# Optimization experiments

Measured on AMD Instinct MI355X. Metric: run time of the kernel, lower is better.

The kernel has to match this reference:

```python
import jax, jax.numpy as jnp
import numpy as np
from jax import lax

B, CIN, HF, WF = 8, 512, 60, 60      # encoder feature
NCLS = 19                            # seg out channels
PATCH = 10                           # patch_size
DEPTH = 8                            # 2**att_depth
UPS = 8                              # seg upsampling
HI = HF * UPS                        # 480 upsampled image size
NP_IMG = (HI // PATCH) ** 2          # 2304 image patches
NP_FEA = (HI // DEPTH // PATCH) ** 2 # 36 feature patches
POOL_SIZES = (1, 2, 3, 6)


def resize_ac(x, H, W):
    # bilinear, align_corners=True (matches F.interpolate/UpsamplingBilinear2d)
    b, c, h, w = x.shape
    ys = jnp.arange(H, dtype=x.dtype) * ((h - 1) / max(H - 1, 1))
    xs = jnp.arange(W, dtype=x.dtype) * ((w - 1) / max(W - 1, 1))
    y0 = jnp.floor(ys).astype(jnp.int32); y1 = jnp.minimum(y0 + 1, h - 1)
    x0 = jnp.floor(xs).astype(jnp.int32); x1 = jnp.minimum(x0 + 1, w - 1)
    wy = (ys - y0.astype(x.dtype))[:, None]
    wx = (xs - x0.astype(x.dtype))[None, :]
    g = lambda yi, xi: x[:, :, yi[:, None], xi[None, :]]
    top = (1 - wx) * g(y0, x0) + wx * g(y0, x1)
    bot = (1 - wx) * g(y1, x0) + wx * g(y1, x1)
    return (1 - wy) * top + wy * bot


def bn_eval(x, gamma, beta, mean, var, eps=1e-5):
    s = lambda v: v[None, :, None, None]
    return (x - s(mean)) * (s(gamma) / jnp.sqrt(s(var) + eps)) + s(beta)


def setup_inputs() -> dict:
    key = jax.random.key(0)
    ks = jax.random.split(key, 16)
    f32 = jnp.float32
    return {
        "feat": jax.random.normal(ks[0], (B, CIN, HF, WF), f32),
        "attentions": jax.random.normal(ks[1], (B, NCLS, NP_IMG, NP_FEA), f32),
        "w_psp": jax.random.normal(ks[2], (4, CIN // 4, CIN), f32) * 0.03,
        "b_psp0": jax.random.normal(ks[3], (CIN // 4,), f32) * 0.02,
        "bn_psp_gamma": jax.random.uniform(ks[4], (3, CIN // 4), f32, 0.5, 1.5),
        "bn_psp_beta": jax.random.normal(ks[5], (3, CIN // 4), f32) * 0.02,
        "bn_psp_mean": jax.random.normal(ks[6], (3, CIN // 4), f32) * 0.02,
        "bn_psp_var": jax.random.uniform(ks[7], (3, CIN // 4), f32, 0.5, 1.5),
        "w_conv": jax.random.normal(ks[8], (512, 2 * CIN), f32) * 0.03,
        "bn_conv_gamma": jax.random.uniform(ks[9], (512,), f32, 0.5, 1.5),
        "bn_conv_beta": jax.random.normal(ks[10], (512,), f32) * 0.02,
        "bn_conv_mean": jax.random.normal(ks[11], (512,), f32) * 0.02,
        "bn_conv_var": jax.random.uniform(ks[12], (512,), f32, 0.5, 1.5),
        "w_segconv": jax.random.normal(ks[13], (NCLS, 512, 3, 3), f32) * 0.03,
        "b_segconv": jax.random.normal(ks[14], (NCLS,), f32) * 0.02,
    }


def _forward(feat, attentions, w_psp, b_psp0, bn_psp_gamma, bn_psp_beta,
             bn_psp_mean, bn_psp_var, w_conv, bn_conv_gamma, bn_conv_beta,
             bn_conv_mean, bn_conv_var, w_segconv, b_segconv):
    # ---- PSP pyramid ----
    branches = []
    for i, p in enumerate(POOL_SIZES):
        k = HF // p
        pooled = feat.reshape(B, CIN, p, k, p, k).mean(axis=(3, 5))  # adaptive avg pool
        y = jnp.einsum('oc,bchw->bohw', w_psp[i], pooled)
        if i == 0:  # pool_size==1 -> no BN, conv has bias
            y = y + b_psp0[None, :, None, None]
        else:
            y = bn_eval(y, bn_psp_gamma[i-1], bn_psp_beta[i-1],
                        bn_psp_mean[i-1], bn_psp_var[i-1])
        y = jax.nn.relu(y)
        branches.append(resize_ac(y, HF, WF))
    x = jnp.concatenate(branches + [feat], axis=1)  # [B, 2*CIN, HF, WF]

    # ---- 1x1 Conv2dReLU + BN (eval), dropout is identity in eval ----
    x = jnp.einsum('oc,bchw->bohw', w_conv, x)
    x = jax.nn.relu(bn_eval(x, bn_conv_gamma, bn_conv_beta, bn_conv_mean, bn_conv_var))

    # ---- SegmentationHead ----
    x = lax.conv_general_dilated(x, w_segconv, (1, 1), 'SAME',
                                 dimension_numbers=('NCHW', 'OIHW', 'NCHW'))
    x = x + b_segconv[None, :, None, None]
    x = resize_ac(x, HI, HI)  # [B, NCLS, 480, 480]

    # one-hot of per-pixel argmax (scatter of ones)
    am = jnp.argmax(x, axis=1)
    x_softmax = (am[:, None] == jnp.arange(NCLS)[None, :, None, None]).astype(x.dtype)

    # grouped ones-conv stride 8 / 64 == 8x8 average pooling
    hf = HI // DEPTH  # 60
    argx_feamap = x_softmax.reshape(B, NCLS, hf, DEPTH, hf, DEPTH).mean(axis=(3, 5))

    # unfold(k=10, s=10): [B, C, 36, 100] (blocks row-major, patch row-major)
    nb = hf // PATCH  # 6
    unf = argx_feamap.reshape(B, NCLS, nb, PATCH, nb, PATCH)
    unf = unf.transpose(0, 1, 2, 4, 3, 5).reshape(B, NCLS, nb * nb, PATCH * PATCH)

    counts = jnp.count_nonzero(attentions, axis=-1, keepdims=True).astype(x.dtype) + 1e-5
    att = jnp.einsum('bcpk,bckq->bcpq', attentions / counts, unf)  # [B,C,2304,100]

    # fold back to [B, C, 480, 480]
    nbi = HI // PATCH  # 48
    corr = att.reshape(B, NCLS, nbi, nbi, PATCH, PATCH)
    corr = corr.transpose(0, 1, 2, 4, 3, 5).reshape(B, NCLS, HI, HI)

    x = corr * x + x  # activation=None -> identity
    return x, attentions


def reference(feat, attentions, w_psp, b_psp0, bn_psp_gamma, bn_psp_beta,
              bn_psp_mean, bn_psp_var, w_conv, bn_conv_gamma, bn_conv_beta,
              bn_conv_mean, bn_conv_var, w_segconv, b_segconv):
    return _forward(feat, attentions, w_psp, b_psp0, bn_psp_gamma, bn_psp_beta,
                    bn_psp_mean, bn_psp_var, w_conv, bn_conv_gamma, bn_conv_beta,
                    bn_conv_mean, bn_conv_var, w_segconv, b_segconv)
```

## Files before the change

### kernel.cpp

```cpp
#include <hip/hip_runtime.h>
#include <stdint.h>

#define NB 8
#define NCLS 19

typedef short s8v __attribute__((ext_vector_type(8)));
typedef float f4v __attribute__((ext_vector_type(4)));

__device__ __forceinline__ unsigned short f2b(float f){
  union { float f; uint32_t u; } v; v.f = f;
  uint32_t u = v.u;
  uint32_t r = (u + 0x7fffu + ((u >> 16) & 1u)) >> 16;
  return (unsigned short)r;
}

#define GLOAD16(g, l) __builtin_amdgcn_global_load_lds( \
    (const __attribute__((address_space(1))) unsigned int*)(g), \
    (__attribute__((address_space(3))) unsigned int*)(l), 16, 0, 0)

#define OFF_X512 0
#define OFF_POOL 31490048
#define OFF_Z    32309248
#define OFF_BNS  33128448
#define OFF_BNB  33130496
#define OFF_SEG  33132544
#define OFF_ARGX 35321344
#define OFF_WSEG 37510144
#define OFF_WF   37805056

__global__ __launch_bounds__(256) void k_setup(
    const float* __restrict__ feat, unsigned short* __restrict__ featT,
    unsigned short* __restrict__ x512p,
    const float* __restrict__ wseg, unsigned short* __restrict__ wsegT,
    const float* __restrict__ wconv, unsigned short* __restrict__ wfT,
    const float* __restrict__ g, const float* __restrict__ be,
    const float* __restrict__ m, const float* __restrict__ v,
    float* __restrict__ sc, float* __restrict__ sh,
    unsigned short* __restrict__ argxT, float* __restrict__ pooled)
{
  __shared__ unsigned short lt[64*528];
  int bid = blockIdx.x;
  if (bid < 456){
    int b = bid / 57, px0 = (bid - b*57)*64;
    for (int i = threadIdx.x; i < 64*512; i += 256){
      int c = i >> 6, px = i & 63;
      float val = feat[((size_t)b*512 + c)*3600 + min(px0+px, 3599)];
      lt[px*528 + c] = f2b(val);
    }
    __syncthreads();
    for (int i = threadIdx.x; i < 4096; i += 256){
      int px = i >> 6, c8 = i & 63;
      s8v vv = *(const s8v*)(lt + px*528 + c8*8);
      *(s8v*)(featT + ((size_t)b*3712 + px0 + px)*512 + c8*8) = vv;
    }
    return;
  }
  bid -= 456;
  if (bid < 488){
    int idx = bid*256 + threadIdx.x;
    if (idx < 124928){
      int pix = idx >> 6;
      int ch  = (idx & 63) << 3;
      int b = pix / 244;
      int r = pix - b*244;
      int h, w;
      if (r < 62){ h = 0; w = r; }
      else if (r < 124){ h = 61; w = r - 62; }
      else if (r < 184){ h = r - 124 + 1; w = 0; }
      else { h = r - 184 + 1; w = 61; }
      s8v z = (s8v){0,0,0,0,0,0,0,0};
      *(s8v*)(x512p + (((size_t)b*62 + h)*62 + w)*512 + ch) = z;
    }
    return;
  }
  bid -= 488;
  if (bid < 576){
    int idx = bid*256 + threadIdx.x;
    if (idx < 9*32*512){
      int tap = idx / (32*512);
      int rem = idx - tap*(32*512);
      int o = rem >> 9, c = rem & 511;
      float val = (o < NCLS) ? wseg[((size_t)o*512 + c)*9 + tap] : 0.0f;
      wsegT[idx] = f2b(val);
    }
    return;
  }
  bid -= 576;
  if (bid < 1024){
    int idx = bid*256 + threadIdx.x;
    if (idx < 512*512){
      int o = idx >> 9, c = idx & 511;
      wfT[idx] = f2b(wconv[(size_t)o*1024 + 512 + c]);
    }
    return;
  }
  bid -= 1024;
  if (bid < 2){
    int i = bid*256 + threadIdx.x;
    if (i < 512){
      float s = g[i] * rsqrtf(v[i] + 1e-5f);
      sc[i] = s; sh[i] = be[i] - m[i]*s;
    }
    return;
  }
  bid -= 2;
  if (bid < 532){
    int gi = bid*256 + threadIdx.x;
    if (gi < 136192){
      s8v z = (s8v){0,0,0,0,0,0,0,0};
      ((s8v*)argxT)[gi] = z;
    }
    return;
  }
  bid -= 532;
  {
    int w = threadIdx.x >> 6, lane = threadIdx.x & 63;
    int bc = bid*4 + w;
    float* rs = (float*)lt + w*64*12;
    if (lane < 60){
      const float* row = feat + (size_t)bc*3600 + lane*60;
      float s6[6];
      #pragma unroll
      for (int j = 0; j < 6; j++){
        float s = 0.f;
        #pragma unroll
        for (int i = 0; i < 10; i++) s += row[j*10+i];
        s6[j] = s;
      }
      float s3_0 = s6[0]+s6[1], s3_1 = s6[2]+s6[3], s3_2 = s6[4]+s6[5];
      float s2_0 = s3_0 + s6[2], s2_1 = s6[3] + s3_2;
      rs[lane*12+0] = s2_0 + s2_1;
      rs[lane*12+1] = s2_0; rs[lane*12+2] = s2_1;
      rs[lane*12+3] = s3_0; rs[lane*12+4] = s3_1; rs[lane*12+5] = s3_2;
      #pragma unroll
      for (int j = 0; j < 6; j++) rs[lane*12+6+j] = s6[j];
    }
    __syncthreads();
    if (lane < 50){
      int P, by, bx, jcol;
      if (lane == 0){ P=1; by=0; bx=0; jcol=0; }
      else if (lane < 5){ P=2; int l=lane-1; by=l>>1; bx=l&1; jcol=1+bx; }
      else if (lane < 14){ P=3; int l=lane-5; by=l/3; bx=l-(l/3)*3; jcol=3+bx; }
      else { P=6; int l=lane-14; by=l/6; bx=l-(l/6)*6; jcol=6+bx; }
      int k = 60/P;
      float s = 0.f;
      for (int rr = 0; rr < k; rr++) s += rs[(by*k+rr)*12 + jcol];
      pooled[(size_t)bc*50 + lane] = s * (1.0f/((float)k*(float)k));
    }
  }
}

__global__ __launch_bounds__(256) void k2_branch(
    const float* __restrict__ pooled, const float* __restrict__ w_psp,
    const float* __restrict__ b_psp0,
    const float* __restrict__ png, const float* __restrict__ pnb,
    const float* __restrict__ pnm, const float* __restrict__ pnv,
    const float* __restrict__ wconv, float* __restrict__ zbuf)
{
  int bin = blockIdx.x % 50;
  int b   = blockIdx.x / 50;
  int br  = (bin < 1) ? 0 : (bin < 5) ? 1 : (bin < 14) ? 2 : 3;
  __shared__ float pl[512];
  __shared__ float ysh[128];
  int t = threadIdx.x;
  pl[t]       = pooled[((size_t)b*512 + t)*50 + bin];
  pl[t + 256] = pooled[((size_t)b*512 + t + 256)*50 + bin];
  __syncthreads();
  if (t < 128){
    const float* wr = w_psp + ((size_t)br*128 + t)*512;
    float s = 0.f;
    #pragma unroll 8
    for (int c = 0; c < 512; c++) s += pl[c]*wr[c];
    if (br == 0) s += b_psp0[t];
    else {
      int ib = (br-1)*128 + t;
      s = (s - pnm[ib]) * png[ib] * rsqrtf(pnv[ib] + 1e-5f) + pnb[ib];
    }
    ysh[t] = fmaxf(s, 0.f);
  }
  __syncthreads();
  for (int o = t; o < 512; o += 256){
    const float* wc = wconv + (size_t)o*1024 + br*128;
    float s = 0.f;
    #pragma unroll
    for (int c = 0; c < 128; c++) s += ysh[c]*wc[c];
    zbuf[((size_t)b*50 + bin)*512 + o] = s;
  }
}

__global__ __launch_bounds__(256) void k3_gemm(
    const unsigned short* __restrict__ featT, const unsigned short* __restrict__ wfT,
    const float* __restrict__ zbuf, const float* __restrict__ bns,
    const float* __restrict__ bnb, unsigned short* __restrict__ x512p)
{
  __shared__ unsigned short lmem[2*128*64];
  unsigned short* lA = lmem;
  unsigned short* lB = lmem + 128*64;

  const int t = threadIdx.x;
  const int lane = t & 63;
  const int wave = t >> 6;
  const int wm = wave >> 1;
  const int wn = wave & 1;
  const int pix0 = blockIdx.x * 128;
  const int o0   = blockIdx.y * 128;
  const int b    = blockIdx.z;

  f4v acc[4][4];
  #pragma unroll
  for (int i = 0; i < 4; i++)
    #pragma unroll
    for (int j = 0; j < 4; j++)
      acc[i][j] = (f4v){0.f,0.f,0.f,0.f};

  const int sub  = lane >> 3;
  const int slot = lane & 7;

  for (int kk = 0; kk < 8; kk++){
    #pragma unroll
    for (int j = 0; j < 4; j++){
      int px = j*32 + wave*8 + sub;
      int pix = min(pix0 + px, 3599);
      const unsigned short* src = featT + ((size_t)b*3712 + pix)*512 + kk*64 + ((slot ^ (px & 7)) << 3);
      GLOAD16(src, lA + j*2048 + wave*512);
    }
    #pragma unroll
    for (int j = 0; j < 4; j++){
      int o = j*32 + wave*8 + sub;
      const unsigned short* src = wfT + (size_t)(o0 + o)*512 + kk*64 + ((slot ^ (o & 7)) << 3);
      GLOAD16(src, lB + j*2048 + wave*512);
    }
    __syncthreads();
    #pragma unroll
    for (int ks = 0; ks < 2; ks++){
      const int chunk = ks*4 + (lane >> 4);
      s8v af[4], bg[4];
      #pragma unroll
      for (int mf = 0; mf < 4; mf++){
        int p = wm*64 + mf*16 + (lane & 15);
        af[mf] = *(s8v*)((char*)lA + p*128 + ((chunk ^ (p & 7)))*16);
      }
      #pragma unroll
      for (int nf = 0; nf < 4; nf++){
        int o = wn*64 + nf*16 + (lane & 15);
        bg[nf] = *(s8v*)((char*)lB + o*128 + ((chunk ^ (o & 7)))*16);
      }
      #pragma unroll
      for (int mf = 0; mf < 4; mf++)
        #pragma unroll
        for (int nf = 0; nf < 4; nf++)
          acc[mf][nf] = __builtin_amdgcn_mfma_f32_16x16x32_bf16(af[mf], bg[nf], acc[mf][nf], 0, 0, 0);
    }
    __syncthreads();
  }

  float* zl  = (float*)lmem;
  float* lsc = zl + 50*128;
  float* lsh = lsc + 128;
  for (int i = t; i < 50*128; i += 256){
    int bin = i >> 7, ol = i & 127;
    zl[i] = zbuf[((size_t)b*50 + bin)*512 + o0 + ol];
  }
  if (t < 128){ lsc[t] = bns[o0 + t]; lsh[t] = bnb[o0 + t]; }
  __syncthreads();

  #pragma unroll
  for (int mf = 0; mf < 4; mf++){
    #pragma unroll
    for (int r = 0; r < 4; r++){
      int p = pix0 + wm*64 + mf*16 + (lane >> 4)*4 + r;
      if (p >= 3600) continue;
      int h = p / 60, w = p - (p/60)*60;
      float wgt[3][4]; int bix[3][4];
      const int pbase[3] = {1,5,14};
      const int psz[3]   = {2,3,6};
      #pragma unroll
      for (int ib = 0; ib < 3; ib++){
        int P = psz[ib];
        float fy = (float)h * (float)(P-1) / 59.0f;
        float fx = (float)w * (float)(P-1) / 59.0f;
        int y0 = (int)fy; int y1 = min(y0+1, P-1); float wy = fy - (float)y0;
        int x0 = (int)fx; int x1 = min(x0+1, P-1); float wx = fx - (float)x0;
        bix[ib][0] = pbase[ib] + y0*P + x0; wgt[ib][0] = (1.f-wy)*(1.f-wx);
        bix[ib][1] = pbase[ib] + y0*P + x1; wgt[ib][1] = (1.f-wy)*wx;
        bix[ib][2] = pbase[ib] + y1*P + x0; wgt[ib][2] = wy*(1.f-wx);
        bix[ib][3] = pbase[ib] + y1*P + x1; wgt[ib][3] = wy*wx;
      }
      size_t obase = (((size_t)b*62 + (h+1))*62 + (w+1))*512 + o0;
      #pragma unroll
      for (int nf = 0; nf < 4; nf++){
        int ol = wn*64 + nf*16 + (lane & 15);
        float zs = zl[ol];
        #pragma unroll
        for (int ib = 0; ib < 3; ib++)
          #pragma unroll
          for (int tp = 0; tp < 4; tp++)
            zs += wgt[ib][tp] * zl[bix[ib][tp]*128 + ol];
        float v = acc[mf][nf][r] + zs;
        v = fmaxf(v * lsc[ol] + lsh[ol], 0.f);
        x512p[obase + ol] = f2b(v);
      }
    }
  }
}

__global__ __launch_bounds__(256) void k4_conv(
    const unsigned short* __restrict__ x512p, const unsigned short* __restrict__ wsegT,
    const float* __restrict__ bseg, float* __restrict__ seg60)
{
  __shared__ unsigned short lW[32*512];
  const int h = blockIdx.x;
  const int b = blockIdx.y;
  const int t = threadIdx.x;
  const int lane = t & 63;
  const int wave = t >> 6;
  const int wpix = wave*16 + (lane & 15);
  const int wld = min(wpix, 59);

  f4v acc[2];
  acc[0] = (f4v){0.f,0.f,0.f,0.f};
  acc[1] = (f4v){0.f,0.f,0.f,0.f};

  for (int tap = 0; tap < 9; tap++){
    __syncthreads();
    for (int i = t; i < 2048; i += 256){
      int orow = i >> 6;
      int cn = i & 63;
      s8v v = *(const s8v*)(wsegT + ((size_t)tap*32 + orow)*512 + cn*8);
      *(s8v*)((char*)lW + orow*1024 + ((cn ^ (orow & 7)))*16) = v;
    }
    __syncthreads();
    int dy = tap/3 - 1, dx = tap - (tap/3)*3 - 1;
    const unsigned short* arow = x512p + (((size_t)b*62 + (h+dy+1))*62 + (wld+dx+1))*512 + (lane>>4)*8;
    #pragma unroll 4
    for (int cs = 0; cs < 16; cs++){
      int cb = cs*32;
      s8v a = *(const s8v*)(arow + cb);
      #pragma unroll
      for (int nf = 0; nf < 2; nf++){
        int o = nf*16 + (lane & 15);
        int chunk = (cb >> 3) + (lane >> 4);
        s8v bv = *(s8v*)((char*)lW + o*1024 + ((chunk ^ (o & 7)))*16);
        acc[nf] = __builtin_amdgcn_mfma_f32_16x16x32_bf16(a, bv, acc[nf], 0, 0, 0);
      }
    }
  }
  #pragma unroll
  for (int nf = 0; nf < 2; nf++){
    int o = nf*16 + (lane & 15);
    if (o < NCLS){
      float bias = bseg[o];
      #pragma unroll
      for (int r = 0; r < 4; r++){
        int wst = wave*16 + (lane >> 4)*4 + r;
        if (wst < 60)
          seg60[(((size_t)b*60 + h)*60 + wst)*NCLS + o] = acc[nf][r] + bias;
      }
    }
  }
}

__global__ __launch_bounds__(256) void k5_argmax(const float* __restrict__ seg60, unsigned short* __restrict__ argxT){
  int fy = blockIdx.x, b = blockIdx.y;
  __shared__ float L[3*60*20];
  int ylo;
  { float yy0 = (float)(fy*8) * (59.0f/479.0f); ylo = (int)yy0; }
  for (int i = threadIdx.x; i < 3600; i += 256){
    int r = i/1200, rem = i - r*1200, x = rem/20, c = rem - x*20;
    int row = min(ylo + r, 59);
    L[i] = (c < 19) ? seg60[(((size_t)b*60 + row)*60 + x)*NCLS + c] : -3.0e38f;
  }
  __syncthreads();
  int wave = threadIdx.x >> 6, lane = threadIdx.x & 63;
  int py = fy*8 + (lane >> 3), lpx = lane & 7;
  float yy = (float)py * (59.0f/479.0f); int y0 = (int)yy; int y1 = min(y0+1, 59); float wy = yy - (float)y0;
  const float* r0 = L + (y0 - ylo)*1200;
  const float* r1 = L + (y1 - ylo)*1200;
  #pragma unroll 3
  for (int pass = 0; pass < 15; pass++){
    int fx = pass*4 + wave;
    int px = fx*8 + lpx;
    float xx = (float)px * (59.0f/479.0f); int x0 = (int)xx; int x1 = min(x0+1, 59); float wx = xx - (float)x0;
    float w00 = (1.f-wy)*(1.f-wx), w01 = (1.f-wy)*wx, w10 = wy*(1.f-wx), w11 = wy*wx;
    const float* s00 = r0 + x0*20; const float* s01 = r0 + x1*20;
    const float* s10 = r1 + x0*20; const float* s11 = r1 + x1*20;
    float best = -3.0e38f; int bc = 0;
    #pragma unroll
    for (int c = 0; c < NCLS; c++){
      float v = w00*s00[c] + w01*s01[c] + w10*s10[c] + w11*s11[c];
      if (v > best){ best = v; bc = c; }
    }
    int cnt = 0;
    #pragma unroll
    for (int c = 0; c < NCLS; c++){
      unsigned long long m = __ballot(bc == c);
      if (lane == c) cnt = __popcll(m);
    }
    int ky = fy/10, qy = fy - (fy/10)*10, kx = fx/10, qx = fx - (fx/10)*10;
    int q = qy*10 + qx, k = ky*6 + kx;
    if (lane < NCLS){
      unsigned short hv = f2b((float)cnt * (1.0f/64.0f));
      argxT[(size_t)(b*NCLS + lane)*7168 + q*64 + (((k>>3) ^ (q&7))<<3) + (k&7)] = hv;
    }
  }
}

__global__ __launch_bounds__(256) void k7_final(
    const float* __restrict__ att, const unsigned short* __restrict__ argxT,
    const float* __restrict__ seg60, float* __restrict__ out, float* __restrict__ out2)
{
  int pr = blockIdx.x, c = blockIdx.y, b = blockIdx.z;
  __shared__ char pool[22720];
  unsigned short* Abf = (unsigned short*)pool;
  unsigned short* Ubf = (unsigned short*)(pool + 6144);
  float* corrl = (float*)pool;
  float* inv   = (float*)(pool + 21504);
  float* srow  = (float*)(pool + 21696);
  const int t = threadIdx.x;
  const int lane = t & 63;
  const int wave = t >> 6;

  int ybase; { float yy0 = (float)(pr*10)*(59.0f/479.0f); ybase = (int)yy0; }

  const size_t aoff = (((size_t)b*NCLS + c)*2304 + (size_t)pr*48)*36;
  const float* ab = att + aoff;
  float* o2 = out2 + aoff;
  for (int i = t; i < 768; i += 256){
    int pc = i >> 4, j = i & 15;
    ushort4 w4 = make_ushort4(0,0,0,0);
    if (j < 9){
      f4v v = *(const f4v*)(ab + pc*36 + j*4);
      *(f4v*)(o2 + pc*36 + j*4) = v;
      w4.x = f2b(v[0]); w4.y = f2b(v[1]); w4.z = f2b(v[2]); w4.w = f2b(v[3]);
    }
    int ch = j >> 1;
    *(ushort4*)((char*)Abf + pc*128 + (((ch ^ (pc & 7)))<<4) + (j & 1)*8) = w4;
  }
  {
    const unsigned short* up = argxT + (size_t)(b*NCLS + c)*7168;
    #pragma unroll
    for (int r = 0; r < 4; r++){
      int chunk0 = r*256 + wave*64;
      if (chunk0 < 896)
        GLOAD16(up + (size_t)(chunk0 + lane)*8, Ubf + (size_t)chunk0*8);
    }
  }
  if (t < 240){
    int j = t/60, x = t - (t/60)*60;
    int row = min(ybase + j, 59);
    srow[j*64 + x] = seg60[(((size_t)b*60 + row)*60 + x)*NCLS + c];
  }
  if (t < 48){
    int nz = 0;
    #pragma unroll
    for (int j2 = 0; j2 < 9; j2++){
      f4v v = *(const f4v*)(ab + t*36 + j2*4);
      nz += (v[0]!=0.f)+(v[1]!=0.f)+(v[2]!=0.f)+(v[3]!=0.f);
    }
    inv[t] = 1.0f/((float)nz + 1e-5f);
  }
  __syncthreads();

  f4v acc[6];
  #pragma unroll
  for (int s = 0; s < 6; s++) acc[s] = (f4v){0.f,0.f,0.f,0.f};
  #pragma unroll
  for (int s = 0; s < 6; s++){
    int pi = wave + s*4;
    if (pi < 21){
      int M = pi/7, N = pi - (pi/7)*7;
      #pragma unroll
      for (int ks = 0; ks < 2; ks++){
        int chunk = ks*4 + (lane >> 4);
        int ar = M*16 + (lane & 15);
        s8v af = *(s8v*)((char*)Abf + ar*128 + ((chunk ^ (ar & 7))<<4));
        int qr = N*16 + (lane & 15);
        s8v bg = *(s8v*)((char*)Ubf + qr*128 + ((chunk ^ (qr & 7))<<4));
        acc[s] = __builtin_amdgcn_mfma_f32_16x16x32_bf16(af, bg, acc[s], 0, 0, 0);
      }
    }
  }
  float hA[4], hB[4];
  {
    float xxa = (float)t * (59.0f/479.0f);
    int xa0 = (int)xxa; int xa1 = min(xa0+1, 59); float wxa = xxa - (float)xa0;
    int px2 = t + 256;
    float xxb = (float)px2 * (59.0f/479.0f);
    int xb0 = (int)xxb; int xb1 = min(xb0+1, 59); float wxb = xxb - (float)xb0;
    #pragma unroll
    for (int j = 0; j < 4; j++){
      hA[j] = (1.f-wxa)*srow[j*64 + xa0] + wxa*srow[j*64 + xa1];
      hB[j] = (px2 < 480) ? ((1.f-wxb)*srow[j*64 + xb0] + wxb*srow[j*64 + xb1]) : 0.f;
    }
  }
  __syncthreads();

  #pragma unroll
  for (int s = 0; s < 6; s++){
    int pi = wave + s*4;
    if (pi < 21){
      int M = pi/7, N = pi - (pi/7)*7;
      int q = N*16 + (lane & 15);
      #pragma unroll
      for (int r = 0; r < 4; r++){
        int pc = M*16 + (lane >> 4)*4 + r;
        corrl[pc*112 + q] = acc[s][r] * inv[pc];
      }
    }
  }
  __syncthreads();

  float* outb = out + ((size_t)b*NCLS + c)*230400 + (size_t)pr*4800;
  int pcA = (t*6554) >> 16, qxA = t - pcA*10;
  int px2 = t + 256;
  int pcB = (px2*6554) >> 16, qxB = px2 - pcB*10;
  #pragma unroll
  for (int qy = 0; qy < 10; qy++){
    int py = pr*10 + qy;
    float yy = (float)py * (59.0f/479.0f);
    int y0 = (int)yy; int y1 = min(y0+1, 59); float wy = yy - (float)y0;
    int j0 = y0 - ybase, j1 = y1 - ybase;
    float h0a = (j0==0)?hA[0]:(j0==1)?hA[1]:(j0==2)?hA[2]:hA[3];
    float h1a = (j1==0)?hA[0]:(j1==1)?hA[1]:(j1==2)?hA[2]:hA[3];
    float omw = 1.f - wy;
    float xv = omw*h0a + wy*h1a;
    outb[qy*480 + t] = xv * (1.f + corrl[pcA*112 + qy*10 + qxA]);
    if (px2 < 480){
      float h0b = (j0==0)?hB[0]:(j0==1)?hB[1]:(j0==2)?hB[2]:hB[3];
      float h1b = (j1==0)?hB[0]:(j1==1)?hB[1]:(j1==2)?hB[2]:hB[3];
      float xv2 = omw*h0b + wy*h1b;
      outb[qy*480 + px2] = xv2 * (1.f + corrl[pcB*112 + qy*10 + qxB]);
    }
  }
}

extern "C" void kernel_launch(void* const* d_in, const int* in_sizes, int n_in,
                              void* d_out, int out_size, void* d_ws, size_t ws_size,
                              hipStream_t stream)
{
  (void)in_sizes; (void)n_in; (void)out_size; (void)ws_size;
  const float* feat   = (const float*)d_in[0];
  const float* attn   = (const float*)d_in[1];
  const float* w_psp  = (const float*)d_in[2];
  const float* b_psp0 = (const float*)d_in[3];
  const float* png    = (const float*)d_in[4];
  const float* pnb    = (const float*)d_in[5];
  const float* pnm    = (const float*)d_in[6];
  const float* pnv    = (const float*)d_in[7];
  const float* wconv  = (const float*)d_in[8];
  const float* cg     = (const float*)d_in[9];
  const float* cbt    = (const float*)d_in[10];
  const float* cm     = (const float*)d_in[11];
  const float* cv     = (const float*)d_in[12];
  const float* wseg   = (const float*)d_in[13];
  const float* bseg   = (const float*)d_in[14];

  float* out1 = (float*)d_out;
  float* out2 = out1 + (size_t)35020800;

  char* ws = (char*)d_ws;
  unsigned short* x512p = (unsigned short*)(ws + OFF_X512);
  float* pooled = (float*)(ws + OFF_POOL);
  float* zbuf   = (float*)(ws + OFF_Z);
  float* bns    = (float*)(ws + OFF_BNS);
  float* bnb    = (float*)(ws + OFF_BNB);
  float* seg60  = (float*)(ws + OFF_SEG);
  unsigned short* argxT = (unsigned short*)(ws + OFF_ARGX);
  unsigned short* wsegT = (unsigned short*)(ws + OFF_WSEG);
  unsigned short* wfT   = (unsigned short*)(ws + OFF_WF);
  unsigned short* featT = (unsigned short*)d_out;

  k_setup<<<4102, 256, 0, stream>>>(feat, featT, x512p, wseg, wsegT, wconv, wfT,
                                    cg, cbt, cm, cv, bns, bnb, argxT, pooled);
  k2_branch<<<400, 256, 0, stream>>>(pooled, w_psp, b_psp0, png, pnb, pnm, pnv, wconv, zbuf);
  k3_gemm<<<dim3(29,4,8), 256, 0, stream>>>(featT, wfT, zbuf, bns, bnb, x512p);
  k4_conv<<<dim3(60,8), 256, 0, stream>>>(x512p, wsegT, bseg, seg60);
  k5_argmax<<<dim3(60,8), 256, 0, stream>>>(seg60, argxT);
  k7_final<<<dim3(48,19,8), 256, 0, stream>>>(attn, argxT, seg60, out1, out2);
}
```

Baseline: 263.4 us.

## Fold pyramid-branch bilinear upsample into GEMM as an extra K block

The per-pixel bilinear combination of the pooled-branch contributions moves out of the k3 epilogue and into the matrix multiply. Precomputed interpolation weights go into an extra 64-wide K slice of featT, and the branch outputs become a bf16 zbufT operand. This removes the LDS staging of a 50x128 float table and the 13-term scalar interpolation per output element. In exchange it adds a ninth K iteration, a wider featT stride, extra setup blocks, and bf16 rounding of the weights and branch values.

```diff
diff --git a/kernel.cpp b/kernel.cpp
--- a/kernel.cpp
+++ b/kernel.cpp
@@ -36,7 +36,8 @@
     const float* __restrict__ g, const float* __restrict__ be,
     const float* __restrict__ m, const float* __restrict__ v,
     float* __restrict__ sc, float* __restrict__ sh,
-    unsigned short* __restrict__ argxT, float* __restrict__ pooled)
+    unsigned short* __restrict__ argxT, unsigned short* __restrict__ zbufT,
+    float* __restrict__ pooled)
 {
   __shared__ unsigned short lt[64*528];
   int bid = blockIdx.x;
@@ -51,7 +52,7 @@
     for (int i = threadIdx.x; i < 4096; i += 256){
       int px = i >> 6, c8 = i & 63;
       s8v vv = *(const s8v*)(lt + px*528 + c8*8);
-      *(s8v*)(featT + ((size_t)b*3712 + px0 + px)*512 + c8*8) = vv;
+      *(s8v*)(featT + ((size_t)b*3712 + px0 + px)*576 + c8*8) = vv;
     }
     return;
   }
@@ -113,6 +114,51 @@
     return;
   }
   bid -= 532;
+  if (bid < 128){
+    int gi = bid*256 + threadIdx.x;
+    if (gi < 32768){
+      s8v z = (s8v){0,0,0,0,0,0,0,0};
+      ((s8v*)zbufT)[gi] = z;
+    }
+    return;
+  }
+  bid -= 128;
+  if (bid < 116){
+    int row = bid*256 + threadIdx.x;
+    if (row < 29696){
+      int b = row / 3712, p = row - b*3712;
+      int pc = min(p, 3599);
+      int h = pc / 60, w = pc - (pc/60)*60;
+      float* wr = (float*)lt + threadIdx.x*64;
+      #pragma unroll
+      for (int i = 0; i < 64; i++) wr[i] = 0.f;
+      wr[0] = 1.0f;
+      const int pbase[3] = {1,5,14};
+      const int psz[3]   = {2,3,6};
+      #pragma unroll
+      for (int ib = 0; ib < 3; ib++){
+        int P = psz[ib];
+        float fy = (float)h * (float)(P-1) / 59.0f;
+        float fx = (float)w * (float)(P-1) / 59.0f;
+        int y0 = (int)fy; int y1 = min(y0+1, P-1); float wy = fy - (float)y0;
+        int x0 = (int)fx; int x1 = min(x0+1, P-1); float wx = fx - (float)x0;
+        wr[pbase[ib] + y0*P + x0] += (1.f-wy)*(1.f-wx);
+        wr[pbase[ib] + y0*P + x1] += (1.f-wy)*wx;
+        wr[pbase[ib] + y1*P + x0] += wy*(1.f-wx);
+        wr[pbase[ib] + y1*P + x1] += wy*wx;
+      }
+      unsigned short* dst = featT + ((size_t)b*3712 + p)*576 + 512;
+      #pragma unroll
+      for (int ch = 0; ch < 8; ch++){
+        s8v vv;
+        #pragma unroll
+        for (int e = 0; e < 8; e++) vv[e] = (short)f2b(wr[ch*8 + e]);
+        *(s8v*)(dst + ch*8) = vv;
+      }
+    }
+    return;
+  }
+  bid -= 116;
   {
     int w = threadIdx.x >> 6, lane = threadIdx.x & 63;
     int bc = bid*4 + w;
@@ -155,7 +201,7 @@
     const float* __restrict__ b_psp0,
     const float* __restrict__ png, const float* __restrict__ pnb,
     const float* __restrict__ pnm, const float* __restrict__ pnv,
-    const float* __restrict__ wconv, float* __restrict__ zbuf)
+    const float* __restrict__ wconv, unsigned short* __restrict__ zbufT)
 {
   int bin = blockIdx.x % 50;
   int b   = blockIdx.x / 50;
@@ -184,13 +230,13 @@
     float s = 0.f;
     #pragma unroll
     for (int c = 0; c < 128; c++) s += ysh[c]*wc[c];
-    zbuf[((size_t)b*50 + bin)*512 + o] = s;
+    zbufT[((size_t)b*512 + o)*64 + bin] = f2b(s);
   }
 }
 
 __global__ __launch_bounds__(256) void k3_gemm(
     const unsigned short* __restrict__ featT, const unsigned short* __restrict__ wfT,
-    const float* __restrict__ zbuf, const float* __restrict__ bns,
+    const unsigned short* __restrict__ zbufT, const float* __restrict__ bns,
     const float* __restrict__ bnb, unsigned short* __restrict__ x512p)
 {
   __shared__ unsigned short lmem[2*128*64];
@@ -216,18 +262,20 @@
   const int sub  = lane >> 3;
   const int slot = lane & 7;
 
-  for (int kk = 0; kk < 8; kk++){
+  for (int kk = 0; kk < 9; kk++){
     #pragma unroll
     for (int j = 0; j < 4; j++){
       int px = j*32 + wave*8 + sub;
       int pix = min(pix0 + px, 3599);
-      const unsigned short* src = featT + ((size_t)b*3712 + pix)*512 + kk*64 + ((slot ^ (px & 7)) << 3);
+      const unsigned short* src = featT + ((size_t)b*3712 + pix)*576 + kk*64 + ((slot ^ (px & 7)) << 3);
       GLOAD16(src, lA + j*2048 + wave*512);
     }
     #pragma unroll
     for (int j = 0; j < 4; j++){
       int o = j*32 + wave*8 + sub;
-      const unsigned short* src = wfT + (size_t)(o0 + o)*512 + kk*64 + ((slot ^ (o & 7)) << 3);
+      const unsigned short* src = (kk < 8)
+        ? wfT + (size_t)(o0 + o)*512 + kk*64 + ((slot ^ (o & 7)) << 3)
+        : zbufT + ((size_t)b*512 + o0 + o)*64 + ((slot ^ (o & 7)) << 3);
       GLOAD16(src, lB + j*2048 + wave*512);
     }
     __syncthreads();
@@ -254,13 +302,8 @@
     __syncthreads();
   }
 
-  float* zl  = (float*)lmem;
-  float* lsc = zl + 50*128;
+  float* lsc = (float*)lmem;
   float* lsh = lsc + 128;
-  for (int i = t; i < 50*128; i += 256){
-    int bin = i >> 7, ol = i & 127;
-    zl[i] = zbuf[((size_t)b*50 + bin)*512 + o0 + ol];
-  }
   if (t < 128){ lsc[t] = bns[o0 + t]; lsh[t] = bnb[o0 + t]; }
   __syncthreads();
 
@@ -271,33 +314,11 @@
       int p = pix0 + wm*64 + mf*16 + (lane >> 4)*4 + r;
       if (p >= 3600) continue;
       int h = p / 60, w = p - (p/60)*60;
-      float wgt[3][4]; int bix[3][4];
-      const int pbase[3] = {1,5,14};
-      const int psz[3]   = {2,3,6};
-      #pragma unroll
-      for (int ib = 0; ib < 3; ib++){
-        int P = psz[ib];
-        float fy = (float)h * (float)(P-1) / 59.0f;
-        float fx = (float)w * (float)(P-1) / 59.0f;
-        int y0 = (int)fy; int y1 = min(y0+1, P-1); float wy = fy - (float)y0;
-        int x0 = (int)fx; int x1 = min(x0+1, P-1); float wx = fx - (float)x0;
-        bix[ib][0] = pbase[ib] + y0*P + x0; wgt[ib][0] = (1.f-wy)*(1.f-wx);
-        bix[ib][1] = pbase[ib] + y0*P + x1; wgt[ib][1] = (1.f-wy)*wx;
-        bix[ib][2] = pbase[ib] + y1*P + x0; wgt[ib][2] = wy*(1.f-wx);
-        bix[ib][3] = pbase[ib] + y1*P + x1; wgt[ib][3] = wy*wx;
-      }
       size_t obase = (((size_t)b*62 + (h+1))*62 + (w+1))*512 + o0;
       #pragma unroll
       for (int nf = 0; nf < 4; nf++){
         int ol = wn*64 + nf*16 + (lane & 15);
-        float zs = zl[ol];
-        #pragma unroll
-        for (int ib = 0; ib < 3; ib++)
-          #pragma unroll
-          for (int tp = 0; tp < 4; tp++)
-            zs += wgt[ib][tp] * zl[bix[ib][tp]*128 + ol];
-        float v = acc[mf][nf][r] + zs;
-        v = fmaxf(v * lsc[ol] + lsh[ol], 0.f);
+        float v = fmaxf(acc[mf][nf][r] * lsc[ol] + lsh[ol], 0.f);
         x512p[obase + ol] = f2b(v);
       }
     }
@@ -561,7 +582,7 @@
   char* ws = (char*)d_ws;
   unsigned short* x512p = (unsigned short*)(ws + OFF_X512);
   float* pooled = (float*)(ws + OFF_POOL);
-  float* zbuf   = (float*)(ws + OFF_Z);
+  unsigned short* zbufT = (unsigned short*)(ws + OFF_Z);
   float* bns    = (float*)(ws + OFF_BNS);
   float* bnb    = (float*)(ws + OFF_BNB);
   float* seg60  = (float*)(ws + OFF_SEG);
@@ -570,10 +591,10 @@
   unsigned short* wfT   = (unsigned short*)(ws + OFF_WF);
   unsigned short* featT = (unsigned short*)d_out;
 
-  k_setup<<<4102, 256, 0, stream>>>(feat, featT, x512p, wseg, wsegT, wconv, wfT,
-                                    cg, cbt, cm, cv, bns, bnb, argxT, pooled);
-  k2_branch<<<400, 256, 0, stream>>>(pooled, w_psp, b_psp0, png, pnb, pnm, pnv, wconv, zbuf);
-  k3_gemm<<<dim3(29,4,8), 256, 0, stream>>>(featT, wfT, zbuf, bns, bnb, x512p);
+  k_setup<<<4346, 256, 0, stream>>>(feat, featT, x512p, wseg, wsegT, wconv, wfT,
+                                    cg, cbt, cm, cv, bns, bnb, argxT, zbufT, pooled);
+  k2_branch<<<400, 256, 0, stream>>>(pooled, w_psp, b_psp0, png, pnb, pnm, pnv, wconv, zbufT);
+  k3_gemm<<<dim3(29,4,8), 256, 0, stream>>>(featT, wfT, zbufT, bns, bnb, x512p);
   k4_conv<<<dim3(60,8), 256, 0, stream>>>(x512p, wsegT, bseg, seg60);
   k5_argmax<<<dim3(60,8), 256, 0, stream>>>(seg60, argxT);
   k7_final<<<dim3(48,19,8), 256, 0, stream>>>(attn, argxT, seg60, out1, out2);
```

New measurement: 246.0 us. -6.6%, faster.
